# Performance work log

Hardware: AMD Instinct MI355X
Metric: run time of the kernel (lower is better)

## Reference

```python
import jax, jax.numpy as jnp
import numpy as np

ALPHA = 0.2
NEG_BIG = -9e15


def setup_inputs() -> dict:
    key = jax.random.key(0)
    k1, k2, k3, k4 = jax.random.split(key, 4)
    N, F_in, F_out = 8192, 512, 128
    h = jax.random.normal(k1, (N, F_in), dtype=jnp.float32)
    adj = jax.random.randint(k2, (N, N), 0, 2, dtype=jnp.int32)
    W = jax.random.normal(k3, (F_in, F_out), dtype=jnp.float32) * 0.05
    a = jax.random.normal(k4, (2 * F_out, 1), dtype=jnp.float32) * 0.05
    return {"h": h, "adj": adj, "W": W, "a": a}


def reference(h, adj, W, a):
    F_out = W.shape[1]
    Wh = h @ W                                  # [N, F_out]
    Wh1 = Wh @ a[:F_out, :]                     # [N, 1]
    Wh2 = Wh @ a[F_out:, :]                     # [N, 1]
    e = Wh1 + Wh2.T                             # [N, N] broadcast add
    e = jnp.where(e >= 0, e, ALPHA * e)         # LeakyReLU
    scores = jnp.where(adj > 0, e, NEG_BIG)     # adjacency mask
    attention = jax.nn.softmax(scores, axis=1)  # row-wise softmax
    h_prime = attention @ Wh                    # [N, F_out]
    return jax.nn.elu(h_prime)                  # concat=True -> elu
```

## Files before the change

### kernel.cpp

```cpp
#include <hip/hip_runtime.h>
#include <stdint.h>

typedef float f32x4 __attribute__((ext_vector_type(4)));
typedef __bf16 bf16x8 __attribute__((ext_vector_type(8)));
typedef unsigned short u16;
typedef unsigned int u32;

#define N_NODES 8192
#define F_IN 512
#define F_OUT 128
#define LRA 0.2f
#define JS 8
#define JLEN (N_NODES / JS)
#define CHUNK 64
#define NCH (JLEN / CHUNK)
#define I_TILE 32

__device__ __forceinline__ u16 f32_to_bf16(float f) {
  union { float f; u32 u; } v; v.f = f;
  u32 u = v.u;
  u += 0x7fffu + ((u >> 16) & 1u);
  return (u16)(u >> 16);
}
__device__ __forceinline__ float dot4(f32x4 a, f32x4 b) {
  return a[0] * b[0] + a[1] * b[1] + a[2] * b[2] + a[3] * b[3];
}

__global__ __launch_bounds__(256) void prep_k(
    const float* __restrict__ W, const float* __restrict__ av,
    u16* __restrict__ WT, float* __restrict__ wa) {
  __shared__ u16 Ts[F_OUT][40];
  const int t = threadIdx.x, kc = (int)blockIdx.x * 32;
  {
    const int k = t >> 3, dof = (t & 7) * 16;
#pragma unroll
    for (int q = 0; q < 4; ++q) {
      f32x4 v = *(const f32x4*)&W[(size_t)(kc + k) * F_OUT + dof + q * 4];
#pragma unroll
      for (int e = 0; e < 4; ++e) Ts[dof + q * 4 + e][k] = f32_to_bf16(v[e]);
    }
  }
  __syncthreads();
  {
    const int d = t >> 1, kh = (t & 1) * 16;
    uint4 o0 = *(uint4*)&Ts[d][kh];
    uint4 o1 = *(uint4*)&Ts[d][kh + 8];
    *(uint4*)&WT[(size_t)d * F_IN + kc + kh] = o0;
    *(uint4*)&WT[(size_t)d * F_IN + kc + kh + 8] = o1;
  }
  {
    const int kl = t >> 3, l8 = t & 7;
    const float* wrow = &W[(size_t)(kc + kl) * F_OUT];
    float s1 = 0.f, s2 = 0.f;
#pragma unroll
    for (int q = 0; q < 2; ++q) {
      int dd = l8 * 16 + q * 8;
      f32x4 w0 = *(const f32x4*)&wrow[dd];
      f32x4 w1 = *(const f32x4*)&wrow[dd + 4];
      s1 += dot4(w0, *(const f32x4*)&av[dd]) + dot4(w1, *(const f32x4*)&av[dd + 4]);
      s2 += dot4(w0, *(const f32x4*)&av[F_OUT + dd]) + dot4(w1, *(const f32x4*)&av[F_OUT + dd + 4]);
    }
#pragma unroll
    for (int m = 1; m <= 4; m <<= 1) {
      s1 += __shfl_xor(s1, m, 64);
      s2 += __shfl_xor(s2, m, 64);
    }
    if (l8 == 0) { wa[kc + kl] = s1; wa[F_IN + kc + kl] = s2; }
  }
}

__global__ __launch_bounds__(256) void gemm_wh(
    const float* __restrict__ h, const u16* __restrict__ WT,
    const float* __restrict__ wa,
    u16* __restrict__ WhT, float* __restrict__ Wh1, float* __restrict__ Wh2) {
  __shared__ u16 Ab[2][32][80];
  __shared__ u16 Bs[2][F_OUT][80];
  const int t = threadIdx.x;
  const int i0 = (int)blockIdx.x * 32;
  const int w = t >> 6, l = t & 63, r = l & 15, oct = l >> 4;
  const int mrow = (w & 1) * 16, ncol = (w >> 1) * 64;
  const int ar = t >> 3, ak = (t & 7) * 8;
  const int br = t >> 1, bk = (t & 1) * 32;

  const float* hrow = &h[(size_t)(i0 + ar) * F_IN + ak];
  const u16* wtrow = &WT[(size_t)br * F_IN + bk];
  const float* wap = &wa[ak];
  const float* wbp = &wa[F_IN + ak];

  f32x4 acc[4];
#pragma unroll
  for (int nf = 0; nf < 4; ++nf) acc[nf] = (f32x4){0.f, 0.f, 0.f, 0.f};
  float s1 = 0.f, s2 = 0.f;

  f32x4 ra0, ra1;
  uint4 rb[4];

#define STORE_A(B)                                                        \
  { u32 p0 = f32_to_bf16(ra0[0]) | ((u32)f32_to_bf16(ra0[1]) << 16);      \
    u32 p1 = f32_to_bf16(ra0[2]) | ((u32)f32_to_bf16(ra0[3]) << 16);      \
    u32 p2 = f32_to_bf16(ra1[0]) | ((u32)f32_to_bf16(ra1[1]) << 16);      \
    u32 p3 = f32_to_bf16(ra1[2]) | ((u32)f32_to_bf16(ra1[3]) << 16);      \
    uint4 v; v.x = p0; v.y = p1; v.z = p2; v.w = p3;                      \
    *(uint4*)&Ab[B][ar][ak] = v; }
#define STORE_B(B)                                                        \
  { *(uint4*)&Bs[B][br][bk + 0]  = rb[0];                                 \
    *(uint4*)&Bs[B][br][bk + 8]  = rb[1];                                 \
    *(uint4*)&Bs[B][br][bk + 16] = rb[2];                                 \
    *(uint4*)&Bs[B][br][bk + 24] = rb[3]; }

  ra0 = *(const f32x4*)&hrow[0];
  ra1 = *(const f32x4*)&hrow[4];
#pragma unroll
  for (int j = 0; j < 4; ++j) rb[j] = *(const uint4*)&wtrow[j * 8];
  s1 += dot4(ra0, *(const f32x4*)&wap[0]) + dot4(ra1, *(const f32x4*)&wap[4]);
  s2 += dot4(ra0, *(const f32x4*)&wbp[0]) + dot4(ra1, *(const f32x4*)&wbp[4]);
  STORE_A(0); STORE_B(0);
  __syncthreads();

#pragma unroll
  for (int it = 0; it < 8; ++it) {
    const int buf = it & 1;
    if (it < 7) {
      const int kc = (it + 1) * 64;
      ra0 = *(const f32x4*)&hrow[kc];
      ra1 = *(const f32x4*)&hrow[kc + 4];
#pragma unroll
      for (int j = 0; j < 4; ++j) rb[j] = *(const uint4*)&wtrow[kc + j * 8];
      s1 += dot4(ra0, *(const f32x4*)&wap[kc]) + dot4(ra1, *(const f32x4*)&wap[kc + 4]);
      s2 += dot4(ra0, *(const f32x4*)&wbp[kc]) + dot4(ra1, *(const f32x4*)&wbp[kc + 4]);
    }
#pragma unroll
    for (int ks = 0; ks < 2; ++ks) {
      bf16x8 af = *(bf16x8*)&Ab[buf][mrow + r][ks * 32 + oct * 8];
#pragma unroll
      for (int nf = 0; nf < 4; ++nf) {
        bf16x8 bfv = *(bf16x8*)&Bs[buf][ncol + nf * 16 + r][ks * 32 + oct * 8];
        acc[nf] = __builtin_amdgcn_mfma_f32_16x16x32_bf16(af, bfv, acc[nf], 0, 0, 0);
      }
    }
    if (it < 7) {
      STORE_A(buf ^ 1); STORE_B(buf ^ 1);
      __syncthreads();
    }
  }
#undef STORE_A
#undef STORE_B

#pragma unroll
  for (int m = 1; m <= 4; m <<= 1) {
    s1 += __shfl_xor(s1, m, 64);
    s2 += __shfl_xor(s2, m, 64);
  }
  if ((t & 7) == 0) { Wh1[i0 + ar] = s1; Wh2[i0 + ar] = s2; }

#pragma unroll
  for (int nf = 0; nf < 4; ++nf) {
    u32 lo = f32_to_bf16(acc[nf][0]) | ((u32)f32_to_bf16(acc[nf][1]) << 16);
    u32 hi = f32_to_bf16(acc[nf][2]) | ((u32)f32_to_bf16(acc[nf][3]) << 16);
    const int d = ncol + nf * 16 + r;
    uint2 v; v.x = lo; v.y = hi;
    *(uint2*)&WhT[(size_t)d * N_NODES + i0 + mrow + oct * 4] = v;
  }
}

__global__ __launch_bounds__(256) void gat_main(
    const int* __restrict__ adj, const float* __restrict__ Wh1,
    const float* __restrict__ Wh2, const u16* __restrict__ WhT,
    float* __restrict__ accp, float* __restrict__ sp) {
  __shared__ __align__(16) u16 Plds[2][I_TILE * CHUNK];
  __shared__ float w2s[JLEN];

  const int t = threadIdx.x;
  const int bi = (int)blockIdx.x / JS;
  const int jsi = (int)blockIdx.x % JS;
  const int i0 = bi * I_TILE;
  const int j0 = jsi * JLEN;
  const int w = t >> 6, l = t & 63, r = l & 15, oct = l >> 4;
  const int il = t >> 3, cg = t & 7;

  for (int k = t * 4; k < JLEN; k += 1024)
    *(f32x4*)&w2s[k] = *(const f32x4*)&Wh2[j0 + k];

  const float cI = Wh1[i0 + il];
  const int* aptr = &adj[(size_t)(i0 + il) * N_NODES + j0 + cg * 8];
  const u32 wb = (u32)(il * (CHUNK * 2)) + (((u32)cg * 16) ^ (((u32)il & 7) << 4));

  const u16* vpt0 = &WhT[(size_t)(w * 32 + r) * N_NODES + j0 + oct * 8];
  const u16* vpt1 = &WhT[(size_t)(w * 32 + 16 + r) * N_NODES + j0 + oct * 8];

  f32x4 acc[2][2];
#pragma unroll
  for (int it = 0; it < 2; ++it)
#pragma unroll
    for (int dt = 0; dt < 2; ++dt) acc[it][dt] = (f32x4){0.f, 0.f, 0.f, 0.f};
  float sden = 0.f;

#define STAGE(a0, a1, CH, B) do {                                           \
    f32x4 wv0 = *(const f32x4*)&w2s[(CH) * CHUNK + cg * 8];                 \
    f32x4 wv1 = *(const f32x4*)&w2s[(CH) * CHUNK + cg * 8 + 4];             \
    u32 pk[4];                                                              \
    _Pragma("unroll")                                                       \
    for (int q = 0; q < 4; ++q) {                                           \
      int aa = (q == 0) ? a0.x : (q == 1) ? a0.z : (q == 2) ? a1.x : a1.z;  \
      int ab = (q == 0) ? a0.y : (q == 1) ? a0.w : (q == 2) ? a1.y : a1.w;  \
      float wA = (q < 2) ? wv0[q * 2] : wv1[(q - 2) * 2];                   \
      float wB = (q < 2) ? wv0[q * 2 + 1] : wv1[(q - 2) * 2 + 1];           \
      float xA = cI + wA; xA = fmaxf(xA, LRA * xA);                         \
      float xB = cI + wB; xB = fmaxf(xB, LRA * xB);                         \
      float pA = aa ? __expf(xA) : 0.f;                                     \
      float pB = ab ? __expf(xB) : 0.f;                                     \
      u32 uA = f32_to_bf16(pA), uB = f32_to_bf16(pB);                       \
      union { u32 u; float f; } fA, fB; fA.u = uA << 16; fB.u = uB << 16;   \
      sden += fA.f + fB.f;                                                  \
      pk[q] = uA | (uB << 16);                                              \
    }                                                                       \
    uint4 pv; pv.x = pk[0]; pv.y = pk[1]; pv.z = pk[2]; pv.w = pk[3];       \
    *(uint4*)((char*)&Plds[B][0] + wb) = pv;                                \
  } while (0)

#define MMA(B, V) do {                                                     \
    _Pragma("unroll")                                                      \
    for (int ks = 0; ks < 2; ++ks) {                                       \
      _Pragma("unroll")                                                    \
      for (int it = 0; it < 2; ++it) {                                     \
        u32 rb_ = (u32)((it * 16 + r) * (CHUNK * 2))                       \
                + (((u32)(oct * 16 + ks * 64)) ^ (((u32)r & 7) << 4));     \
        bf16x8 af = *(bf16x8*)((char*)&Plds[B][0] + rb_);                  \
        acc[it][0] = __builtin_amdgcn_mfma_f32_16x16x32_bf16(af, V[ks], acc[it][0], 0, 0, 0);     \
        acc[it][1] = __builtin_amdgcn_mfma_f32_16x16x32_bf16(af, V[2 + ks], acc[it][1], 0, 0, 0); \
      }                                                                    \
    }                                                                      \
  } while (0)

  int4 aE0, aE1, aO0, aO1;
  bf16x8 vc[4], vn[4];

  aE0 = *(const int4*)(aptr + 0);
  aE1 = *(const int4*)(aptr + 4);
  aO0 = *(const int4*)(aptr + CHUNK);
  aO1 = *(const int4*)(aptr + CHUNK + 4);
  vc[0] = *(const bf16x8*)(vpt0 + 0);
  vc[1] = *(const bf16x8*)(vpt0 + 32);
  vc[2] = *(const bf16x8*)(vpt1 + 0);
  vc[3] = *(const bf16x8*)(vpt1 + 32);
  __syncthreads();
  STAGE(aE0, aE1, 0, 0);
  __syncthreads();

#pragma unroll 1
  for (int ch = 0; ch < NCH; ch += 2) {
    if (ch + 2 < NCH) {
      aE0 = *(const int4*)(aptr + (ch + 2) * CHUNK);
      aE1 = *(const int4*)(aptr + (ch + 2) * CHUNK + 4);
    }
    vn[0] = *(const bf16x8*)(vpt0 + (ch + 1) * CHUNK);
    vn[1] = *(const bf16x8*)(vpt0 + (ch + 1) * CHUNK + 32);
    vn[2] = *(const bf16x8*)(vpt1 + (ch + 1) * CHUNK);
    vn[3] = *(const bf16x8*)(vpt1 + (ch + 1) * CHUNK + 32);
    MMA(0, vc);
    STAGE(aO0, aO1, ch + 1, 1);
    __syncthreads();

    if (ch + 3 < NCH) {
      aO0 = *(const int4*)(aptr + (ch + 3) * CHUNK);
      aO1 = *(const int4*)(aptr + (ch + 3) * CHUNK + 4);
    }
    if (ch + 2 < NCH) {
      vc[0] = *(const bf16x8*)(vpt0 + (ch + 2) * CHUNK);
      vc[1] = *(const bf16x8*)(vpt0 + (ch + 2) * CHUNK + 32);
      vc[2] = *(const bf16x8*)(vpt1 + (ch + 2) * CHUNK);
      vc[3] = *(const bf16x8*)(vpt1 + (ch + 2) * CHUNK + 32);
    }
    MMA(1, vn);
    if (ch + 2 < NCH) {
      STAGE(aE0, aE1, ch + 2, 0);
      __syncthreads();
    }
  }
#undef STAGE
#undef MMA

  {
    float s = sden;
    s += __shfl_xor(s, 1, 64);
    s += __shfl_xor(s, 2, 64);
    s += __shfl_xor(s, 4, 64);
    if ((l & 7) == 0) sp[(size_t)jsi * N_NODES + i0 + il] = s;
  }

  float* ap = &accp[((size_t)jsi * N_NODES + i0 + oct * 4) * F_OUT + w * 32 + r];
#pragma unroll
  for (int it = 0; it < 2; ++it)
#pragma unroll
    for (int dt = 0; dt < 2; ++dt)
#pragma unroll
      for (int rr = 0; rr < 4; ++rr)
        ap[(size_t)(it * 16 + rr) * F_OUT + dt * 16] = acc[it][dt][rr];
}

__global__ __launch_bounds__(256) void finalize_k(
    const float* __restrict__ accp, const float* __restrict__ sp,
    float* __restrict__ out) {
  const int vidx = (int)blockIdx.x * 256 + threadIdx.x;
  const int i = vidx >> 5;
  f32x4 num = (f32x4){0.f, 0.f, 0.f, 0.f};
  float den = 0.f;
#pragma unroll
  for (int s = 0; s < JS; ++s) {
    num += *((const f32x4*)accp + (size_t)s * (N_NODES * F_OUT / 4) + vidx);
    den += sp[(size_t)s * N_NODES + i];
  }
  f32x4 o;
#pragma unroll
  for (int c = 0; c < 4; ++c) {
    float x = num[c] / den;
    o[c] = x > 0.f ? x : expm1f(x);
  }
  *((f32x4*)out + vidx) = o;
}

extern "C" void kernel_launch(void* const* d_in, const int* in_sizes, int n_in,
                              void* d_out, int out_size, void* d_ws, size_t ws_size,
                              hipStream_t stream) {
  const float* h = (const float*)d_in[0];
  const int* adj = (const int*)d_in[1];
  const float* W = (const float*)d_in[2];
  const float* av = (const float*)d_in[3];
  float* out = (float*)d_out;
  char* ws = (char*)d_ws;

  u16* WT = (u16*)ws;
  float* wa = (float*)(ws + (256ull << 10));
  u16* WhT = (u16*)(ws + (512ull << 10));
  float* Wh1 = (float*)(ws + (512ull << 10) + (2ull << 20));
  float* Wh2 = (float*)(ws + (512ull << 10) + (2ull << 20) + (32ull << 10));
  float* sp = (float*)(ws + (512ull << 10) + (2ull << 20) + (64ull << 10));
  float* accp = (float*)(ws + (512ull << 10) + (2ull << 20) + (320ull << 10));

  prep_k<<<16, 256, 0, stream>>>(W, av, WT, wa);
  gemm_wh<<<N_NODES / 32, 256, 0, stream>>>(h, WT, wa, WhT, Wh1, Wh2);
  gat_main<<<(N_NODES / I_TILE) * JS, 256, 0, stream>>>(adj, Wh1, Wh2, WhT, accp, sp);
  finalize_k<<<(N_NODES * F_OUT) / 1024, 256, 0, stream>>>(accp, sp, out);
}
```

Baseline: 118.7 us.

## Pack adjacency into bitmask in separate pass and halve j-splits

Adds a pack_adj kernel that turns the int32 adjacency matrix into a 1-bit-per-edge bitmask. gat_main then loads each tile's mask words into shared memory once instead of streaming int4 adjacency values inside the chunk loop. The j-split count drops from 8 to 4, which halves the partial accumulators written and reduced by finalize. The full 256MB adjacency is still read once by the pack pass, and gat_main now has fewer blocks, more LDS per block and longer loops per block.

```diff
diff --git a/kernel.cpp b/kernel.cpp
--- a/kernel.cpp
+++ b/kernel.cpp
@@ -10,11 +10,12 @@
 #define F_IN 512
 #define F_OUT 128
 #define LRA 0.2f
-#define JS 8
+#define JS 4
 #define JLEN (N_NODES / JS)
 #define CHUNK 64
 #define NCH (JLEN / CHUNK)
 #define I_TILE 32
+#define NWORDS (N_NODES / 32)
 
 __device__ __forceinline__ u16 f32_to_bf16(float f) {
   union { float f; u32 u; } v; v.f = f;
@@ -24,6 +25,22 @@
 }
 __device__ __forceinline__ float dot4(f32x4 a, f32x4 b) {
   return a[0] * b[0] + a[1] * b[1] + a[2] * b[2] + a[3] * b[3];
+}
+
+__global__ __launch_bounds__(256) void pack_adj(
+    const int* __restrict__ adj, u32* __restrict__ bm) {
+  const size_t wi = (size_t)blockIdx.x * 256 + threadIdx.x;
+  const int* p = adj + wi * 32;
+  u32 m = 0;
+#pragma unroll
+  for (int q = 0; q < 8; ++q) {
+    int4 v = *(const int4*)(p + q * 4);
+    m |= (v.x ? 1u : 0u) << (q * 4);
+    m |= (v.y ? 1u : 0u) << (q * 4 + 1);
+    m |= (v.z ? 1u : 0u) << (q * 4 + 2);
+    m |= (v.w ? 1u : 0u) << (q * 4 + 3);
+  }
+  bm[wi] = m;
 }
 
 __global__ __launch_bounds__(256) void prep_k(
@@ -164,11 +181,12 @@
 }
 
 __global__ __launch_bounds__(256) void gat_main(
-    const int* __restrict__ adj, const float* __restrict__ Wh1,
+    const u32* __restrict__ bm, const float* __restrict__ Wh1,
     const float* __restrict__ Wh2, const u16* __restrict__ WhT,
     float* __restrict__ accp, float* __restrict__ sp) {
   __shared__ __align__(16) u16 Plds[2][I_TILE * CHUNK];
   __shared__ float w2s[JLEN];
+  __shared__ u32 mlds[I_TILE][JLEN / 32];
 
   const int t = threadIdx.x;
   const int bi = (int)blockIdx.x / JS;
@@ -180,10 +198,18 @@
 
   for (int k = t * 4; k < JLEN; k += 1024)
     *(f32x4*)&w2s[k] = *(const f32x4*)&Wh2[j0 + k];
+  {
+    const u32* bmrow = &bm[(size_t)(i0 + il) * NWORDS + (j0 >> 5)];
+    uint4 m0 = *(const uint4*)(bmrow + cg * 8);
+    uint4 m1 = *(const uint4*)(bmrow + cg * 8 + 4);
+    *(uint4*)&mlds[il][cg * 8] = m0;
+    *(uint4*)&mlds[il][cg * 8 + 4] = m1;
+  }
 
   const float cI = Wh1[i0 + il];
-  const int* aptr = &adj[(size_t)(i0 + il) * N_NODES + j0 + cg * 8];
   const u32 wb = (u32)(il * (CHUNK * 2)) + (((u32)cg * 16) ^ (((u32)il & 7) << 4));
+  const int msh = (cg & 3) * 8;
+  const int mwi = cg >> 2;
 
   const u16* vpt0 = &WhT[(size_t)(w * 32 + r) * N_NODES + j0 + oct * 8];
   const u16* vpt1 = &WhT[(size_t)(w * 32 + 16 + r) * N_NODES + j0 + oct * 8];
@@ -195,20 +221,19 @@
     for (int dt = 0; dt < 2; ++dt) acc[it][dt] = (f32x4){0.f, 0.f, 0.f, 0.f};
   float sden = 0.f;
 
-#define STAGE(a0, a1, CH, B) do {                                           \
+#define STAGE(CH, B) do {                                                   \
+    u32 mb = mlds[il][(CH) * 2 + mwi] >> msh;                               \
     f32x4 wv0 = *(const f32x4*)&w2s[(CH) * CHUNK + cg * 8];                 \
     f32x4 wv1 = *(const f32x4*)&w2s[(CH) * CHUNK + cg * 8 + 4];             \
     u32 pk[4];                                                              \
     _Pragma("unroll")                                                       \
     for (int q = 0; q < 4; ++q) {                                           \
-      int aa = (q == 0) ? a0.x : (q == 1) ? a0.z : (q == 2) ? a1.x : a1.z;  \
-      int ab = (q == 0) ? a0.y : (q == 1) ? a0.w : (q == 2) ? a1.y : a1.w;  \
       float wA = (q < 2) ? wv0[q * 2] : wv1[(q - 2) * 2];                   \
       float wB = (q < 2) ? wv0[q * 2 + 1] : wv1[(q - 2) * 2 + 1];           \
       float xA = cI + wA; xA = fmaxf(xA, LRA * xA);                         \
       float xB = cI + wB; xB = fmaxf(xB, LRA * xB);                         \
-      float pA = aa ? __expf(xA) : 0.f;                                     \
-      float pB = ab ? __expf(xB) : 0.f;                                     \
+      float pA = (mb & (1u << (2 * q))) ? __expf(xA) : 0.f;                 \
+      float pB = (mb & (2u << (2 * q))) ? __expf(xB) : 0.f;                 \
       u32 uA = f32_to_bf16(pA), uB = f32_to_bf16(pB);                       \
       union { u32 u; float f; } fA, fB; fA.u = uA << 16; fB.u = uB << 16;   \
       sden += fA.f + fB.f;                                                  \
@@ -232,39 +257,26 @@
     }                                                                      \
   } while (0)
 
-  int4 aE0, aE1, aO0, aO1;
   bf16x8 vc[4], vn[4];
 
-  aE0 = *(const int4*)(aptr + 0);
-  aE1 = *(const int4*)(aptr + 4);
-  aO0 = *(const int4*)(aptr + CHUNK);
-  aO1 = *(const int4*)(aptr + CHUNK + 4);
   vc[0] = *(const bf16x8*)(vpt0 + 0);
   vc[1] = *(const bf16x8*)(vpt0 + 32);
   vc[2] = *(const bf16x8*)(vpt1 + 0);
   vc[3] = *(const bf16x8*)(vpt1 + 32);
   __syncthreads();
-  STAGE(aE0, aE1, 0, 0);
+  STAGE(0, 0);
   __syncthreads();
 
 #pragma unroll 1
   for (int ch = 0; ch < NCH; ch += 2) {
-    if (ch + 2 < NCH) {
-      aE0 = *(const int4*)(aptr + (ch + 2) * CHUNK);
-      aE1 = *(const int4*)(aptr + (ch + 2) * CHUNK + 4);
-    }
     vn[0] = *(const bf16x8*)(vpt0 + (ch + 1) * CHUNK);
     vn[1] = *(const bf16x8*)(vpt0 + (ch + 1) * CHUNK + 32);
     vn[2] = *(const bf16x8*)(vpt1 + (ch + 1) * CHUNK);
     vn[3] = *(const bf16x8*)(vpt1 + (ch + 1) * CHUNK + 32);
     MMA(0, vc);
-    STAGE(aO0, aO1, ch + 1, 1);
+    STAGE(ch + 1, 1);
     __syncthreads();
 
-    if (ch + 3 < NCH) {
-      aO0 = *(const int4*)(aptr + (ch + 3) * CHUNK);
-      aO1 = *(const int4*)(aptr + (ch + 3) * CHUNK + 4);
-    }
     if (ch + 2 < NCH) {
       vc[0] = *(const bf16x8*)(vpt0 + (ch + 2) * CHUNK);
       vc[1] = *(const bf16x8*)(vpt0 + (ch + 2) * CHUNK + 32);
@@ -273,7 +285,7 @@
     }
     MMA(1, vn);
     if (ch + 2 < NCH) {
-      STAGE(aE0, aE1, ch + 2, 0);
+      STAGE(ch + 2, 0);
       __syncthreads();
     }
   }
@@ -329,16 +341,18 @@
   float* out = (float*)d_out;
   char* ws = (char*)d_ws;
 
-  u16* WT = (u16*)ws;
-  float* wa = (float*)(ws + (256ull << 10));
-  u16* WhT = (u16*)(ws + (512ull << 10));
-  float* Wh1 = (float*)(ws + (512ull << 10) + (2ull << 20));
-  float* Wh2 = (float*)(ws + (512ull << 10) + (2ull << 20) + (32ull << 10));
-  float* sp = (float*)(ws + (512ull << 10) + (2ull << 20) + (64ull << 10));
-  float* accp = (float*)(ws + (512ull << 10) + (2ull << 20) + (320ull << 10));
-
+  u32* bm = (u32*)ws;
+  u16* WT = (u16*)(ws + (8ull << 20));
+  float* wa = (float*)(ws + (8ull << 20) + (128ull << 10));
+  u16* WhT = (u16*)(ws + (9ull << 20));
+  float* Wh1 = (float*)(ws + (11ull << 20));
+  float* Wh2 = (float*)(ws + (11ull << 20) + (32ull << 10));
+  float* sp = (float*)(ws + (11ull << 20) + (64ull << 10));
+  float* accp = (float*)(ws + (11ull << 20) + (256ull << 10));
+
+  pack_adj<<<(N_NODES * N_NODES / 32) / 256, 256, 0, stream>>>(adj, bm);
   prep_k<<<16, 256, 0, stream>>>(W, av, WT, wa);
   gemm_wh<<<N_NODES / 32, 256, 0, stream>>>(h, WT, wa, WhT, Wh1, Wh2);
-  gat_main<<<(N_NODES / I_TILE) * JS, 256, 0, stream>>>(adj, Wh1, Wh2, WhT, accp, sp);
+  gat_main<<<(N_NODES / I_TILE) * JS, 256, 0, stream>>>(bm, Wh1, Wh2, WhT, accp, sp);
   finalize_k<<<(N_NODES * F_OUT) / 1024, 256, 0, stream>>>(accp, sp, out);
 }
```

Result: slower. 147.2 us (+24.1%).
